# Kernel optimization log

Hardware: AMD Instinct MI355X
Metric: run time of the kernel (lower is better)

Reference implementation:

```python
import jax, jax.numpy as jnp
import numpy as np

N_NODES = 200000
N_EDGES = 6400000
IN_CH = 256
HID = 16


def gcn_conv(h, src, dst, deg_inv_sqrt, W, b, n_nodes):
    """One GCNConv (PyG semantics: add self-loops, symmetric norm, linear, scatter-add, bias)."""
    hw = h @ W  # [N, out]
    norm = deg_inv_sqrt[src] * deg_inv_sqrt[dst]  # [E]
    agg = jax.ops.segment_sum(norm[:, None] * hw[src], dst, num_segments=n_nodes)
    # self-loop contribution: deg_inv_sqrt[i]^2 * hw[i]
    agg = agg + hw * (deg_inv_sqrt ** 2)[:, None]
    return agg + b


def setup_inputs() -> dict:
    key = jax.random.key(0)
    k_x, k_e, k_w1, k_w2, k_w3 = jax.random.split(key, 5)
    x = jax.random.normal(k_x, (N_NODES, IN_CH), dtype=jnp.float32)
    edge_index = jax.random.randint(k_e, (2, N_EDGES), 0, N_NODES, dtype=jnp.int64)
    # Glorot-ish init for the three GCNConv weights, zeros for biases (PyG default)
    W1 = jax.random.normal(k_w1, (IN_CH, HID), dtype=jnp.float32) * (1.0 / np.sqrt(IN_CH))
    b1 = jnp.zeros((HID,), dtype=jnp.float32)
    W2 = jax.random.normal(k_w2, (HID, HID), dtype=jnp.float32) * (1.0 / np.sqrt(HID))
    b2 = jnp.zeros((HID,), dtype=jnp.float32)
    W3 = jax.random.normal(k_w3, (HID, 1), dtype=jnp.float32) * (1.0 / np.sqrt(HID))
    b3 = jnp.zeros((1,), dtype=jnp.float32)
    return {"x": x, "edge_index": edge_index, "W1": W1, "b1": b1,
            "W2": W2, "b2": b2, "W3": W3, "b3": b3}


def reference(x, edge_index, W1, b1, W2, b2, W3, b3):
    n_nodes = x.shape[0]
    src, dst = edge_index[0], edge_index[1]
    # GCN norm with self-loops: deg counts incoming edges + 1 self-loop
    deg = jax.ops.segment_sum(jnp.ones_like(dst, dtype=x.dtype), dst,
                              num_segments=n_nodes) + 1.0
    deg_inv_sqrt = deg ** -0.5  # deg >= 1, safe
    h = jax.nn.relu(gcn_conv(x, src, dst, deg_inv_sqrt, W1, b1, n_nodes))
    # dropout is identity in eval mode
    h = jax.nn.relu(gcn_conv(h, src, dst, deg_inv_sqrt, W2, b2, n_nodes))
    out = gcn_conv(h, src, dst, deg_inv_sqrt, W3, b3, n_nodes)  # [N, 1]
    return out
```

## Files before the change

### kernel.cpp

```cpp
#include <hip/hip_runtime.h>

#define NN 200000
#define EE 6400000L
#define NCB 196
#define CAP 36864
#define TILE 8192
#define NTILE 782

__device__ inline void f4add(float4& a, const float4 v) {
    a.x += v.x; a.y += v.y; a.z += v.z; a.w += v.w;
}

union SMem {
    struct {
        unsigned lv[TILE];
        unsigned char lb[TILE];
        int lh[NCB], lseg[NCB], lcur[NCB];
    } p;
    float wl[256 * 16];
};

__global__ void k_detect(const int* __restrict__ w, int* __restrict__ flag,
                         int* __restrict__ gcur) {
    __shared__ int any;
    if (threadIdx.x == 0) any = 0;
    __syncthreads();
    int found = 0;
    for (int i = threadIdx.x; i < 8192; i += 256)
        if (w[2 * i + 1] != 0) found = 1;
    if (found) atomicOr(&any, 1);
    if (threadIdx.x < NCB) gcur[threadIdx.x] = threadIdx.x * CAP;
    __syncthreads();
    if (threadIdx.x == 0) flag[0] = any ? 0 : 1;
}

__global__ __launch_bounds__(256) void k_fused(
    const int* __restrict__ ew, const int* __restrict__ flag,
    int* __restrict__ gcur, unsigned* __restrict__ stage,
    const float* __restrict__ x, const float* __restrict__ W1,
    float4* __restrict__ hw1, long e, int n) {
    __shared__ SMem sm;
    int t = threadIdx.x;
    int role = blockIdx.x & 1;
    int idx = blockIdx.x >> 1;

    if (role == 0) {
        for (int i = t; i < NCB; i += 256) { sm.p.lh[i] = 0; sm.p.lcur[i] = 0; }
        __syncthreads();
        long t0 = (long)idx * TILE;
        int cnt = (int)min((long)TILE, e - t0);
        int shift = *flag;
        for (int i = t; i < cnt; i += 256) {
            int s = ew[(t0 + i) << shift];
            int d = ew[(EE + t0 + i) << shift];
            int b = d >> 10;
            sm.p.lv[i] = (unsigned)s | ((unsigned)(d & 1023) << 18);
            sm.p.lb[i] = (unsigned char)b;
            atomicAdd(&sm.p.lh[b], 1);
        }
        __syncthreads();
        for (int i = t; i < NCB; i += 256)
            if (sm.p.lh[i]) sm.p.lseg[i] = atomicAdd(&gcur[i], sm.p.lh[i]);
        __syncthreads();
        for (int i = t; i < cnt; i += 256) {
            int b = sm.p.lb[i];
            int r = atomicAdd(&sm.p.lcur[b], 1);
            stage[sm.p.lseg[b] + r] = sm.p.lv[i];
        }
    } else {
#pragma unroll
        for (int i = 0; i < 4; ++i)
            ((float4*)sm.wl)[t + i * 256] = ((const float4*)W1)[t + i * 256];
        __syncthreads();
        int node = idx * 256 + t;
        if (node >= n) return;
        const float4* xr = (const float4*)(x + (long)node * 256);
        float acc[16];
#pragma unroll
        for (int o = 0; o < 16; ++o) acc[o] = 0.f;
#pragma unroll 8
        for (int kk = 0; kk < 64; ++kk) {
            float4 xv = xr[kk];
#pragma unroll
            for (int q = 0; q < 4; ++q) {
                float xs = (q == 0) ? xv.x : (q == 1) ? xv.y : (q == 2) ? xv.z : xv.w;
                const float4* wr = (const float4*)&sm.wl[(kk * 4 + q) * 16];
#pragma unroll
                for (int oo = 0; oo < 4; ++oo) {
                    float4 wv = wr[oo];
                    acc[oo * 4 + 0] = fmaf(xs, wv.x, acc[oo * 4 + 0]);
                    acc[oo * 4 + 1] = fmaf(xs, wv.y, acc[oo * 4 + 1]);
                    acc[oo * 4 + 2] = fmaf(xs, wv.z, acc[oo * 4 + 2]);
                    acc[oo * 4 + 3] = fmaf(xs, wv.w, acc[oo * 4 + 3]);
                }
            }
        }
#pragma unroll
        for (int q = 0; q < 4; ++q)
            hw1[(long)node * 4 + q] = make_float4(acc[q * 4], acc[q * 4 + 1],
                                                  acc[q * 4 + 2], acc[q * 4 + 3]);
    }
}

__global__ __launch_bounds__(1024) void k_sortB(
    const unsigned* __restrict__ stage, const int* __restrict__ gcur,
    float* __restrict__ dis, int2* __restrict__ odn,
    unsigned* __restrict__ csr, float4* __restrict__ hw1, int n) {
    __shared__ int cnt[1024];
    __shared__ int cur[1024];
    __shared__ int wsum[16];
    int t = threadIdx.x, B = blockIdx.x;
    cnt[t] = 0;
    __syncthreads();
    int s0 = B * CAP, s1 = gcur[B];
    for (int i = s0 + t; i < s1; i += 1024)
        atomicAdd(&cnt[stage[i] >> 18], 1);
    __syncthreads();
    int c = cnt[t];
    int pc = (c + 3) & ~3;
    int lane = t & 63, w = t >> 6;
    int s = pc;
#pragma unroll
    for (int o = 1; o < 64; o <<= 1) {
        int u = __shfl_up(s, o, 64);
        if (lane >= o) s += u;
    }
    if (lane == 63) wsum[w] = s;
    __syncthreads();
    int add = 0;
    for (int k = 0; k < w; ++k) add += wsum[k];
    int excl = s - pc + add;
    cur[t] = excl;
    int node = B * 1024 + t;
    if (node < n) {
        float dv = rsqrtf((float)(c + 1));
        odn[node] = make_int2(s0 + excl, c);
        dis[node] = dv;
        float4* row = hw1 + (long)node * 4;
#pragma unroll
        for (int q = 0; q < 4; ++q) {
            float4 v = row[q];
            row[q] = make_float4(v.x * dv, v.y * dv, v.z * dv, v.w * dv);
        }
    }
    __syncthreads();
    for (int i = s0 + t; i < s1; i += 1024) {
        unsigned v = stage[i];
        int pos = s0 + atomicAdd(&cur[v >> 18], 1);
        csr[pos] = v & 0x3FFFF;
    }
}

__global__ __launch_bounds__(256) void k_g16a(
    const int2* __restrict__ odn, const unsigned* __restrict__ csr,
    const float* __restrict__ dis, const float4* __restrict__ tab,
    const float* __restrict__ b1v, const float* __restrict__ W2,
    float4* __restrict__ out2) {
    __shared__ float h1s[64 * 17];
    __shared__ float W2l[256];
    int t = threadIdx.x;
    if (t < 64) ((float4*)W2l)[t] = ((const float4*)W2)[t];
    int node = blockIdx.x * 64 + (t >> 2);
    int j = t & 3;
    int2 od = odn[node];
    int s0 = od.x, dg = od.y;
    float4 aA = make_float4(0.f, 0.f, 0.f, 0.f);
    float4 aB = make_float4(0.f, 0.f, 0.f, 0.f);
    int k = 0;
    for (; k + 8 <= dg; k += 8) {
        uint4 eL = *(const uint4*)(csr + s0 + k);
        uint4 eH = *(const uint4*)(csr + s0 + k + 4);
        f4add(aA, tab[eL.x * 4 + j]);
        f4add(aB, tab[eH.x * 4 + j]);
        f4add(aA, tab[eL.y * 4 + j]);
        f4add(aB, tab[eH.y * 4 + j]);
        f4add(aA, tab[eL.z * 4 + j]);
        f4add(aB, tab[eH.z * 4 + j]);
        f4add(aA, tab[eL.w * 4 + j]);
        f4add(aB, tab[eH.w * 4 + j]);
    }
    if (k + 4 <= dg) {
        uint4 e = *(const uint4*)(csr + s0 + k);
        f4add(aA, tab[e.x * 4 + j]);
        f4add(aB, tab[e.y * 4 + j]);
        f4add(aA, tab[e.z * 4 + j]);
        f4add(aB, tab[e.w * 4 + j]);
        k += 4;
    }
    for (; k < dg; ++k)
        f4add(aA, tab[csr[s0 + k] * 4 + j]);
    f4add(aA, aB);
    f4add(aA, tab[node * 4 + j]);
    float dv = dis[node];
    float4 bb = ((const float4*)b1v)[j];
    float4 r = make_float4(fmaf(dv, aA.x, bb.x), fmaf(dv, aA.y, bb.y),
                           fmaf(dv, aA.z, bb.z), fmaf(dv, aA.w, bb.w));
    r.x = fmaxf(r.x, 0.f); r.y = fmaxf(r.y, 0.f);
    r.z = fmaxf(r.z, 0.f); r.w = fmaxf(r.w, 0.f);
    int nl = t >> 2;
    h1s[nl * 17 + 4 * j + 0] = r.x;
    h1s[nl * 17 + 4 * j + 1] = r.y;
    h1s[nl * 17 + 4 * j + 2] = r.z;
    h1s[nl * 17 + 4 * j + 3] = r.w;
    __syncthreads();
    float4 acc = make_float4(0.f, 0.f, 0.f, 0.f);
#pragma unroll
    for (int kk = 0; kk < 16; ++kk) {
        float hv = h1s[nl * 17 + kk];
        float4 wv = ((const float4*)&W2l[kk * 16])[j];
        acc.x = fmaf(hv, wv.x, acc.x);
        acc.y = fmaf(hv, wv.y, acc.y);
        acc.z = fmaf(hv, wv.z, acc.z);
        acc.w = fmaf(hv, wv.w, acc.w);
    }
    out2[(long)node * 4 + j] = make_float4(acc.x * dv, acc.y * dv,
                                           acc.z * dv, acc.w * dv);
}

__global__ __launch_bounds__(256) void k_g16b(
    const int2* __restrict__ odn, const unsigned* __restrict__ csr,
    const float* __restrict__ dis, const float4* __restrict__ tab,
    const float* __restrict__ b2v, const float* __restrict__ W3,
    float* __restrict__ hws3) {
    int t = threadIdx.x;
    int node = blockIdx.x * 64 + (t >> 2);
    int j = t & 3;
    int2 od = odn[node];
    int s0 = od.x, dg = od.y;
    float4 aA = make_float4(0.f, 0.f, 0.f, 0.f);
    float4 aB = make_float4(0.f, 0.f, 0.f, 0.f);
    int k = 0;
    for (; k + 8 <= dg; k += 8) {
        uint4 eL = *(const uint4*)(csr + s0 + k);
        uint4 eH = *(const uint4*)(csr + s0 + k + 4);
        f4add(aA, tab[eL.x * 4 + j]);
        f4add(aB, tab[eH.x * 4 + j]);
        f4add(aA, tab[eL.y * 4 + j]);
        f4add(aB, tab[eH.y * 4 + j]);
        f4add(aA, tab[eL.z * 4 + j]);
        f4add(aB, tab[eH.z * 4 + j]);
        f4add(aA, tab[eL.w * 4 + j]);
        f4add(aB, tab[eH.w * 4 + j]);
    }
    if (k + 4 <= dg) {
        uint4 e = *(const uint4*)(csr + s0 + k);
        f4add(aA, tab[e.x * 4 + j]);
        f4add(aB, tab[e.y * 4 + j]);
        f4add(aA, tab[e.z * 4 + j]);
        f4add(aB, tab[e.w * 4 + j]);
        k += 4;
    }
    for (; k < dg; ++k)
        f4add(aA, tab[csr[s0 + k] * 4 + j]);
    f4add(aA, aB);
    f4add(aA, tab[node * 4 + j]);
    float dv = dis[node];
    float4 bb = ((const float4*)b2v)[j];
    float4 r = make_float4(fmaf(dv, aA.x, bb.x), fmaf(dv, aA.y, bb.y),
                           fmaf(dv, aA.z, bb.z), fmaf(dv, aA.w, bb.w));
    r.x = fmaxf(r.x, 0.f); r.y = fmaxf(r.y, 0.f);
    r.z = fmaxf(r.z, 0.f); r.w = fmaxf(r.w, 0.f);
    float4 w3 = ((const float4*)W3)[j];
    float pd = r.x * w3.x + r.y * w3.y + r.z * w3.z + r.w * w3.w;
    pd += __shfl_xor(pd, 1, 4);
    pd += __shfl_xor(pd, 2, 4);
    if (j == 0) hws3[node] = pd * dv;
}

__global__ __launch_bounds__(256) void k_g1(
    const int2* __restrict__ odn, const unsigned* __restrict__ csr,
    const float* __restrict__ dis, const float* __restrict__ hws3,
    const float* __restrict__ b, float* __restrict__ out, int n) {
    int t = threadIdx.x;
    int node = blockIdx.x * 16 + (t >> 4);
    int ln = t & 15;
    if (node >= n) return;
    int2 od = odn[node];
    int s0 = od.x, dg = od.y;
    float acc = 0.f;
    for (int k = ln; k < dg; k += 16)
        acc += hws3[csr[s0 + k]];
#pragma unroll
    for (int o = 8; o >= 1; o >>= 1) acc += __shfl_down(acc, o, 16);
    if (ln == 0)
        out[node] = fmaf(dis[node], acc + hws3[node], b[0]);
}

extern "C" void kernel_launch(void* const* d_in, const int* in_sizes, int n_in,
                              void* d_out, int out_size, void* d_ws, size_t ws_size,
                              hipStream_t stream) {
    const float* x  = (const float*)d_in[0];
    const int*   ew = (const int*)d_in[1];
    const float* W1 = (const float*)d_in[2];
    const float* b1 = (const float*)d_in[3];
    const float* W2 = (const float*)d_in[4];
    const float* b2 = (const float*)d_in[5];
    const float* W3 = (const float*)d_in[6];
    const float* b3 = (const float*)d_in[7];
    float* out = (float*)d_out;

    unsigned* stage = (unsigned*)d_ws;
    unsigned* csr   = stage + (long)NCB * CAP;
    int*      gcur  = (int*)(csr + (long)NCB * CAP);
    int*      flag  = gcur + 256;
    int2*     odn   = (int2*)(flag + 16);
    float*    dis   = (float*)(odn + 200704);
    float4*   bufA  = (float4*)(dis + 200704);
    float4*   bufB  = bufA + 4 * 200064;

    const int n = NN;
    const long e = EE;
    int gb = n / 64;
    int g1b = n / 16;

    k_detect<<<1, 256, 0, stream>>>(ew, flag, gcur);
    k_fused<<<2 * NTILE, 256, 0, stream>>>(ew, flag, gcur, stage, x, W1, bufA, e, n);
    k_sortB<<<NCB, 1024, 0, stream>>>(stage, gcur, dis, odn, csr, bufA, n);
    k_g16a<<<gb, 256, 0, stream>>>(odn, csr, dis, bufA, b1, W2, bufB);
    k_g16b<<<gb, 256, 0, stream>>>(odn, csr, dis, bufB, b2, W3, (float*)bufA);
    k_g1<<<g1b, 256, 0, stream>>>(odn, csr, dis, (const float*)bufA, b3, out, n);
}
```

Before: 439.9 us.

## Split fused bin/matmul kernel and apply degree scaling in matmul epilogue

```diff
diff --git a/kernel.cpp b/kernel.cpp
--- a/kernel.cpp
+++ b/kernel.cpp
@@ -11,15 +11,6 @@
     a.x += v.x; a.y += v.y; a.z += v.z; a.w += v.w;
 }
 
-union SMem {
-    struct {
-        unsigned lv[TILE];
-        unsigned char lb[TILE];
-        int lh[NCB], lseg[NCB], lcur[NCB];
-    } p;
-    float wl[256 * 16];
-};
-
 __global__ void k_detect(const int* __restrict__ w, int* __restrict__ flag,
                          int* __restrict__ gcur) {
     __shared__ int any;
@@ -34,78 +25,40 @@
     if (threadIdx.x == 0) flag[0] = any ? 0 : 1;
 }
 
-__global__ __launch_bounds__(256) void k_fused(
+__global__ __launch_bounds__(256) void k_passA(
     const int* __restrict__ ew, const int* __restrict__ flag,
-    int* __restrict__ gcur, unsigned* __restrict__ stage,
-    const float* __restrict__ x, const float* __restrict__ W1,
-    float4* __restrict__ hw1, long e, int n) {
-    __shared__ SMem sm;
-    int t = threadIdx.x;
-    int role = blockIdx.x & 1;
-    int idx = blockIdx.x >> 1;
-
-    if (role == 0) {
-        for (int i = t; i < NCB; i += 256) { sm.p.lh[i] = 0; sm.p.lcur[i] = 0; }
-        __syncthreads();
-        long t0 = (long)idx * TILE;
-        int cnt = (int)min((long)TILE, e - t0);
-        int shift = *flag;
-        for (int i = t; i < cnt; i += 256) {
-            int s = ew[(t0 + i) << shift];
-            int d = ew[(EE + t0 + i) << shift];
-            int b = d >> 10;
-            sm.p.lv[i] = (unsigned)s | ((unsigned)(d & 1023) << 18);
-            sm.p.lb[i] = (unsigned char)b;
-            atomicAdd(&sm.p.lh[b], 1);
-        }
-        __syncthreads();
-        for (int i = t; i < NCB; i += 256)
-            if (sm.p.lh[i]) sm.p.lseg[i] = atomicAdd(&gcur[i], sm.p.lh[i]);
-        __syncthreads();
-        for (int i = t; i < cnt; i += 256) {
-            int b = sm.p.lb[i];
-            int r = atomicAdd(&sm.p.lcur[b], 1);
-            stage[sm.p.lseg[b] + r] = sm.p.lv[i];
-        }
-    } else {
-#pragma unroll
-        for (int i = 0; i < 4; ++i)
-            ((float4*)sm.wl)[t + i * 256] = ((const float4*)W1)[t + i * 256];
-        __syncthreads();
-        int node = idx * 256 + t;
-        if (node >= n) return;
-        const float4* xr = (const float4*)(x + (long)node * 256);
-        float acc[16];
-#pragma unroll
-        for (int o = 0; o < 16; ++o) acc[o] = 0.f;
-#pragma unroll 8
-        for (int kk = 0; kk < 64; ++kk) {
-            float4 xv = xr[kk];
-#pragma unroll
-            for (int q = 0; q < 4; ++q) {
-                float xs = (q == 0) ? xv.x : (q == 1) ? xv.y : (q == 2) ? xv.z : xv.w;
-                const float4* wr = (const float4*)&sm.wl[(kk * 4 + q) * 16];
-#pragma unroll
-                for (int oo = 0; oo < 4; ++oo) {
-                    float4 wv = wr[oo];
-                    acc[oo * 4 + 0] = fmaf(xs, wv.x, acc[oo * 4 + 0]);
-                    acc[oo * 4 + 1] = fmaf(xs, wv.y, acc[oo * 4 + 1]);
-                    acc[oo * 4 + 2] = fmaf(xs, wv.z, acc[oo * 4 + 2]);
-                    acc[oo * 4 + 3] = fmaf(xs, wv.w, acc[oo * 4 + 3]);
-                }
-            }
-        }
-#pragma unroll
-        for (int q = 0; q < 4; ++q)
-            hw1[(long)node * 4 + q] = make_float4(acc[q * 4], acc[q * 4 + 1],
-                                                  acc[q * 4 + 2], acc[q * 4 + 3]);
+    int* __restrict__ gcur, unsigned* __restrict__ stage, long e) {
+    __shared__ unsigned lv[TILE];
+    __shared__ unsigned char lb[TILE];
+    __shared__ int lh[NCB], lseg[NCB], lcur[NCB];
+    for (int i = threadIdx.x; i < NCB; i += 256) { lh[i] = 0; lcur[i] = 0; }
+    __syncthreads();
+    long t0 = (long)blockIdx.x * TILE;
+    int cnt = (int)min((long)TILE, e - t0);
+    int shift = *flag;
+    for (int i = threadIdx.x; i < cnt; i += 256) {
+        int s = ew[(t0 + i) << shift];
+        int d = ew[(EE + t0 + i) << shift];
+        int b = d >> 10;
+        lv[i] = (unsigned)s | ((unsigned)(d & 1023) << 18);
+        lb[i] = (unsigned char)b;
+        atomicAdd(&lh[b], 1);
+    }
+    __syncthreads();
+    for (int i = threadIdx.x; i < NCB; i += 256)
+        if (lh[i]) lseg[i] = atomicAdd(&gcur[i], lh[i]);
+    __syncthreads();
+    for (int i = threadIdx.x; i < cnt; i += 256) {
+        int b = lb[i];
+        int r = atomicAdd(&lcur[b], 1);
+        stage[lseg[b] + r] = lv[i];
     }
 }
 
 __global__ __launch_bounds__(1024) void k_sortB(
     const unsigned* __restrict__ stage, const int* __restrict__ gcur,
     float* __restrict__ dis, int2* __restrict__ odn,
-    unsigned* __restrict__ csr, float4* __restrict__ hw1, int n) {
+    unsigned* __restrict__ csr, int n) {
     __shared__ int cnt[1024];
     __shared__ int cur[1024];
     __shared__ int wsum[16];
@@ -133,15 +86,8 @@
     cur[t] = excl;
     int node = B * 1024 + t;
     if (node < n) {
-        float dv = rsqrtf((float)(c + 1));
         odn[node] = make_int2(s0 + excl, c);
-        dis[node] = dv;
-        float4* row = hw1 + (long)node * 4;
-#pragma unroll
-        for (int q = 0; q < 4; ++q) {
-            float4 v = row[q];
-            row[q] = make_float4(v.x * dv, v.y * dv, v.z * dv, v.w * dv);
-        }
+        dis[node] = rsqrtf((float)(c + 1));
     }
     __syncthreads();
     for (int i = s0 + t; i < s1; i += 1024) {
@@ -149,6 +95,48 @@
         int pos = s0 + atomicAdd(&cur[v >> 18], 1);
         csr[pos] = v & 0x3FFFF;
     }
+}
+
+__global__ __launch_bounds__(256) void k_mm1(
+    const float* __restrict__ x, const float* __restrict__ W,
+    const float* __restrict__ dis, float4* __restrict__ outr, int n) {
+    __shared__ float Wl[256 * 16];
+    int t = threadIdx.x;
+#pragma unroll
+    for (int i = 0; i < 4; ++i)
+        ((float4*)Wl)[t + i * 256] = ((const float4*)W)[t + i * 256];
+    __syncthreads();
+
+    int node = blockIdx.x * 256 + t;
+    if (node >= n) return;
+
+    const float4* xr = (const float4*)(x + (long)node * 256);
+    float acc[16];
+#pragma unroll
+    for (int o = 0; o < 16; ++o) acc[o] = 0.f;
+
+#pragma unroll 8
+    for (int kk = 0; kk < 64; ++kk) {
+        float4 xv = xr[kk];
+#pragma unroll
+        for (int q = 0; q < 4; ++q) {
+            float xs = (q == 0) ? xv.x : (q == 1) ? xv.y : (q == 2) ? xv.z : xv.w;
+            const float4* wr = (const float4*)&Wl[(kk * 4 + q) * 16];
+#pragma unroll
+            for (int oo = 0; oo < 4; ++oo) {
+                float4 wv = wr[oo];
+                acc[oo * 4 + 0] = fmaf(xs, wv.x, acc[oo * 4 + 0]);
+                acc[oo * 4 + 1] = fmaf(xs, wv.y, acc[oo * 4 + 1]);
+                acc[oo * 4 + 2] = fmaf(xs, wv.z, acc[oo * 4 + 2]);
+                acc[oo * 4 + 3] = fmaf(xs, wv.w, acc[oo * 4 + 3]);
+            }
+        }
+    }
+    float dv = dis[node];
+#pragma unroll
+    for (int q = 0; q < 4; ++q)
+        outr[node * 4 + q] = make_float4(acc[q * 4] * dv, acc[q * 4 + 1] * dv,
+                                         acc[q * 4 + 2] * dv, acc[q * 4 + 3] * dv);
 }
 
 __global__ __launch_bounds__(256) void k_g16a(
@@ -310,12 +298,14 @@
 
     const int n = NN;
     const long e = EE;
+    int nb = (n + 255) / 256;
     int gb = n / 64;
     int g1b = n / 16;
 
     k_detect<<<1, 256, 0, stream>>>(ew, flag, gcur);
-    k_fused<<<2 * NTILE, 256, 0, stream>>>(ew, flag, gcur, stage, x, W1, bufA, e, n);
-    k_sortB<<<NCB, 1024, 0, stream>>>(stage, gcur, dis, odn, csr, bufA, n);
+    k_passA<<<NTILE, 256, 0, stream>>>(ew, flag, gcur, stage, e);
+    k_sortB<<<NCB, 1024, 0, stream>>>(stage, gcur, dis, odn, csr, n);
+    k_mm1<<<nb, 256, 0, stream>>>(x, W1, dis, bufA, n);
     k_g16a<<<gb, 256, 0, stream>>>(odn, csr, dis, bufA, b1, W2, bufB);
     k_g16b<<<gb, 256, 0, stream>>>(odn, csr, dis, bufB, b2, W3, (float*)bufA);
     k_g1<<<g1b, 256, 0, stream>>>(odn, csr, dis, (const float*)bufA, b3, out, n);
```

Result: no change. 433.8 us (-1.4%).
